# Kernel optimization log

Hardware: AMD Instinct MI355X
Metric: run time of the kernel (lower is better)

The kernel has to match this reference:

```python
import jax, jax.numpy as jnp
import numpy as np


def setup_inputs() -> dict:
    key = jax.random.key(0)
    k1, k2, k3, k4 = jax.random.split(key, 4)
    S, B = 64000, 64
    audio = jax.random.normal(k1, (S, B), dtype=jnp.float32)
    g = jax.random.uniform(k2, (S, B, 1), dtype=jnp.float32)
    twoR = jax.random.uniform(k3, (S, B, 1), dtype=jnp.float32)
    mix = jax.random.uniform(k4, (S, B, 3), dtype=jnp.float32)
    return {"audio": audio, "g": g, "twoR": twoR, "mix": mix}


def reference(audio, g, twoR, mix):
    # audio: [S, B]; g, twoR: [S, B, 1]; mix: [S, B, 3]
    S, B = audio.shape
    T = 1.0 / (1.0 + g * (g + twoR))                      # [S, B, 1]
    ones = jnp.ones_like(g)
    # Time-varying 2x2 transition matrix H[t, b] = T * [[1, -g], [g, 2Rg+1]]
    H = T[..., None] * jnp.concatenate(
        [ones, -g, g, twoR * g + 1.0], axis=-1).reshape(S, B, 2, 2)
    gHB = g * T * jnp.concatenate([ones, g], axis=-1)     # [S, B, 2]
    gHBx = gHB * audio[..., None]                         # [S, B, 2]

    def step(state, inp):
        # state: [B, 2]; Ht: [B, 2, 2]; bt: [B, 2]
        Ht, bt = inp
        Yt = bt + jnp.einsum('bij,bj->bi', Ht, state)
        return 2.0 * Yt - state, Yt

    state0 = jnp.ones((B, 2), dtype=audio.dtype)
    _, Y = jax.lax.scan(step, state0, (H, gHBx))          # Y: [S, B, 2]

    twoR2 = twoR[..., 0]                                  # [S, B]
    y_hps = audio - twoR2 * Y[..., 0] - Y[..., 1]
    y_mixed = (twoR2 * mix[..., 0] * Y[..., 0]
               + mix[..., 1] * Y[..., 1]
               + mix[..., 2] * y_hps)
    return y_mixed.T                                      # [B, S]
```

## Files before the change

kernel.cpp:

```cpp
#include <hip/hip_runtime.h>

#define S_LEN  64000
#define B_N    64
#define MCH    8
#define WPB    8
#define BSTEPS (MCH * WPB)
#define NBLK   (S_LEN / BSTEPS)
#define SC_T   1024

struct Aff { float m00, m01, m10, m11, v0, v1; };

__device__ __forceinline__ Aff aff_id() {
    Aff r; r.m00 = 1.f; r.m01 = 0.f; r.m10 = 0.f; r.m11 = 1.f; r.v0 = 0.f; r.v1 = 0.f;
    return r;
}

__device__ __forceinline__ Aff aff_comp(const Aff& X, const Aff& Y) {
    Aff r;
    r.m00 = fmaf(X.m00, Y.m00, X.m01 * Y.m10);
    r.m01 = fmaf(X.m00, Y.m01, X.m01 * Y.m11);
    r.m10 = fmaf(X.m10, Y.m00, X.m11 * Y.m10);
    r.m11 = fmaf(X.m10, Y.m01, X.m11 * Y.m11);
    r.v0  = fmaf(X.m00, Y.v0, fmaf(X.m01, Y.v1, X.v0));
    r.v1  = fmaf(X.m10, Y.v0, fmaf(X.m11, Y.v1, X.v1));
    return r;
}

__device__ __forceinline__ Aff svf_step(float g, float R, float x) {
    Aff a;
    float T  = 1.0f / fmaf(g, g + R, 1.0f);
    float gT = g * T;
    a.m00 = fmaf(2.0f, T, -1.0f);
    a.m01 = -2.0f * gT;
    a.m10 =  2.0f * gT;
    a.m11 = fmaf(2.0f, fmaf(R, gT, T), -1.0f);
    a.v0  = a.m10 * x;
    a.v1  = g * a.v0;
    return a;
}

__device__ __forceinline__ void aff_store_lds(float* p, const Aff& a) {
    p[0] = a.m00; p[1] = a.m01; p[2] = a.m10; p[3] = a.m11; p[4] = a.v0; p[5] = a.v1;
}
__device__ __forceinline__ Aff aff_load_lds(const float* p) {
    Aff a; a.m00 = p[0]; a.m01 = p[1]; a.m10 = p[2]; a.m11 = p[3]; a.v0 = p[4]; a.v1 = p[5];
    return a;
}
__device__ __forceinline__ void aff_store_g4(float4* p, const Aff& a) {
    p[0] = make_float4(a.m00, a.m01, a.m10, a.m11);
    p[1] = make_float4(a.v0,  a.v1,  0.f,   0.f);
}
__device__ __forceinline__ Aff aff_load_g4(const float4* p) {
    float4 x = p[0], y = p[1];
    Aff a; a.m00 = x.x; a.m01 = x.y; a.m10 = x.z; a.m11 = x.w; a.v0 = y.x; a.v1 = y.y;
    return a;
}

__global__ __launch_bounds__(512, 4) void k_macro(
    const float* __restrict__ audio, const float* __restrict__ g,
    const float* __restrict__ twoR, float4* __restrict__ wsMac)
{
    __shared__ float affs[WPB * B_N * 7];
    const int b   = threadIdx.x & 63;
    const int w   = threadIdx.x >> 6;
    const int blk = blockIdx.x;
    const int base = (blk * BSTEPS + w * MCH) * B_N + b;

    Aff acc = aff_id();
#pragma unroll
    for (int i = 0; i < MCH; ++i) {
        const int idx = base + i * B_N;
        acc = aff_comp(svf_step(g[idx], twoR[idx], audio[idx]), acc);
    }
    aff_store_lds(&affs[(w * B_N + b) * 7], acc);
    __syncthreads();

    if (w == 0) {
        Aff M = acc;
#pragma unroll
        for (int j = 1; j < WPB; ++j) {
            Aff A = aff_load_lds(&affs[(j * B_N + b) * 7]);
            M = aff_comp(A, M);
        }
        aff_store_g4(&wsMac[((long)b * NBLK + blk) * 2], M);
    }
}

__global__ __launch_bounds__(SC_T, 2) void k_scan(
    const float4* __restrict__ wsMac, float2* __restrict__ sIn)
{
    const int b    = blockIdx.x;
    const int t    = threadIdx.x;
    const int lane = t & 63;
    const int wave = t >> 6;

    Aff m = (t < NBLK) ? aff_load_g4(&wsMac[((long)b * NBLK + t) * 2]) : aff_id();

    Aff acc = m;
#pragma unroll
    for (int d = 1; d < 64; d <<= 1) {
        Aff o;
        o.m00 = __shfl_up(acc.m00, (unsigned)d, 64);
        o.m01 = __shfl_up(acc.m01, (unsigned)d, 64);
        o.m10 = __shfl_up(acc.m10, (unsigned)d, 64);
        o.m11 = __shfl_up(acc.m11, (unsigned)d, 64);
        o.v0  = __shfl_up(acc.v0,  (unsigned)d, 64);
        o.v1  = __shfl_up(acc.v1,  (unsigned)d, 64);
        if (lane >= d) acc = aff_comp(acc, o);
    }

    __shared__ Aff wt[SC_T / 64];
    if (lane == 63) wt[wave] = acc;
    __syncthreads();

    if (wave == 0 && lane < 16) {
        Aff a = wt[lane];
#pragma unroll
        for (int d = 1; d < 16; d <<= 1) {
            Aff o;
            o.m00 = __shfl_up(a.m00, (unsigned)d, 64);
            o.m01 = __shfl_up(a.m01, (unsigned)d, 64);
            o.m10 = __shfl_up(a.m10, (unsigned)d, 64);
            o.m11 = __shfl_up(a.m11, (unsigned)d, 64);
            o.v0  = __shfl_up(a.v0,  (unsigned)d, 64);
            o.v1  = __shfl_up(a.v1,  (unsigned)d, 64);
            if (lane >= d) a = aff_comp(a, o);
        }
        wt[lane] = a;
    }
    __syncthreads();

    if (t < NBLK) {
        Aff E;
        E.m00 = __shfl_up(acc.m00, 1u, 64);
        E.m01 = __shfl_up(acc.m01, 1u, 64);
        E.m10 = __shfl_up(acc.m10, 1u, 64);
        E.m11 = __shfl_up(acc.m11, 1u, 64);
        E.v0  = __shfl_up(acc.v0,  1u, 64);
        E.v1  = __shfl_up(acc.v1,  1u, 64);
        if (lane == 0) E = aff_id();
        if (wave > 0) E = aff_comp(E, wt[wave - 1]);

        float e0 = E.m00 + E.m01 + E.v0;
        float e1 = E.m10 + E.m11 + E.v1;
        sIn[t * B_N + b] = make_float2(e0, e1);
    }
}

__global__ __launch_bounds__(512, 4) void k_replay(
    const float* __restrict__ audio, const float* __restrict__ g,
    const float* __restrict__ twoR, const float* __restrict__ mix,
    const float2* __restrict__ sIn, float* __restrict__ out)
{
    __shared__ float lds[BSTEPS * 65];
    const int b   = threadIdx.x & 63;
    const int w   = threadIdx.x >> 6;
    const int blk = blockIdx.x;
    const int base = (blk * BSTEPS + w * MCH) * B_N + b;

    const float3* mix3 = (const float3*)mix;
    float gv[MCH], Rv[MCH], xv[MCH];
    float3 mv[MCH];
#pragma unroll
    for (int i = 0; i < MCH; ++i) {
        const int idx = base + i * B_N;
        gv[i] = g[idx]; Rv[i] = twoR[idx]; xv[i] = audio[idx];
        mv[i] = mix3[idx];
    }

    Aff acc = aff_id();
#pragma unroll
    for (int i = 0; i < MCH; ++i)
        acc = aff_comp(svf_step(gv[i], Rv[i], xv[i]), acc);
    aff_store_lds(&lds[(w * B_N + b) * 7], acc);
    __syncthreads();

    float2 sm = sIn[blk * B_N + b];
    Aff P = aff_id();
    for (int j = 0; j < w; ++j) {
        Aff A = aff_load_lds(&lds[(j * B_N + b) * 7]);
        P = aff_comp(A, P);
    }
    float s0 = fmaf(P.m00, sm.x, fmaf(P.m01, sm.y, P.v0));
    float s1 = fmaf(P.m10, sm.x, fmaf(P.m11, sm.y, P.v1));
    __syncthreads();

#pragma unroll
    for (int i = 0; i < MCH; ++i) {
        float gg = gv[i], R = Rv[i], x = xv[i];
        float T  = 1.0f / fmaf(gg, gg + R, 1.0f);
        float gT = gg * T;
        float b0 = gT * x;
        float b1 = gg * b0;
        float Y0 = fmaf(T, s0, fmaf(-gT, s1, b0));
        float Y1 = fmaf(gT, s0, fmaf(fmaf(R, gT, T), s1, b1));
        s0 = fmaf(2.0f, Y0, -s0);
        s1 = fmaf(2.0f, Y1, -s1);

        float yh = x - fmaf(R, Y0, Y1);
        float y  = fmaf(R * mv[i].x, Y0, fmaf(mv[i].y, Y1, mv[i].z * yh));

        lds[(w * MCH + i) * 65 + b] = y;
    }
    __syncthreads();

    const int col = threadIdx.x & 63;
    const int r0  = threadIdx.x >> 6;
    const int colbase = blk * BSTEPS;
#pragma unroll
    for (int r = r0; r < B_N; r += WPB) {
        out[r * S_LEN + colbase + col] = lds[col * 65 + r];
    }
}

extern "C" void kernel_launch(void* const* d_in, const int* in_sizes, int n_in,
                              void* d_out, int out_size, void* d_ws, size_t ws_size,
                              hipStream_t stream)
{
    const float* audio = (const float*)d_in[0];
    const float* g     = (const float*)d_in[1];
    const float* twoR  = (const float*)d_in[2];
    const float* mix   = (const float*)d_in[3];
    float* out = (float*)d_out;

    float4* wsMac = (float4*)d_ws;
    float2* sIn   = (float2*)(wsMac + (long)B_N * NBLK * 2);

    k_macro <<<dim3(NBLK), dim3(512), 0, stream>>>(audio, g, twoR, wsMac);
    k_scan  <<<dim3(B_N), dim3(SC_T), 0, stream>>>(wsMac, sIn);
    k_replay<<<dim3(NBLK), dim3(512), 0, stream>>>(audio, g, twoR, mix, sIn, out);
}
```

Measured before the change: 37.08 us.

## Coarsen macro blocks to 128 steps and derive half-block states in scan

The macro kernel now covers 128 timesteps per block, with each lane handling two batch columns through float2 loads. It also records a half-block prefix transform, so the scan kernel produces boundary states at 64-step granularity while scanning only 500 macro elements per batch. This halves the macro grid and cuts the scan length. The cost is extra workspace traffic for the half transforms and more serial composition work in wave 0 of the macro kernel.

```diff
diff --git a/kernel.cpp b/kernel.cpp
--- a/kernel.cpp
+++ b/kernel.cpp
@@ -3,9 +3,12 @@
 #define S_LEN  64000
 #define B_N    64
 #define MCH    8
-#define WPB    8
-#define BSTEPS (MCH * WPB)
-#define NBLK   (S_LEN / BSTEPS)
+#define CPB    16
+#define BSTEPS (MCH * CPB)
+#define NMAC   (S_LEN / BSTEPS)
+#define RSTEPS 64
+#define NREP   (S_LEN / RSTEPS)
+#define RWPB   8
 #define SC_T   1024
 
 struct Aff { float m00, m01, m10, m11, v0, v1; };
@@ -58,43 +61,56 @@
 
 __global__ __launch_bounds__(512, 4) void k_macro(
     const float* __restrict__ audio, const float* __restrict__ g,
-    const float* __restrict__ twoR, float4* __restrict__ wsMac)
-{
-    __shared__ float affs[WPB * B_N * 7];
-    const int b   = threadIdx.x & 63;
-    const int w   = threadIdx.x >> 6;
-    const int blk = blockIdx.x;
-    const int base = (blk * BSTEPS + w * MCH) * B_N + b;
-
-    Aff acc = aff_id();
+    const float* __restrict__ twoR, float4* __restrict__ wsMac,
+    float4* __restrict__ wsHalf)
+{
+    __shared__ float affs[CPB * B_N * 7];
+    const int lane = threadIdx.x & 63;
+    const int w    = threadIdx.x >> 6;
+    const int j2   = lane & 31;
+    const int h    = lane >> 5;
+    const int c    = w * 2 + h;
+    const int blk  = blockIdx.x;
+    const int base = (blk * BSTEPS + c * MCH) * B_N + 2 * j2;
+
+    Aff accA = aff_id(), accB = aff_id();
 #pragma unroll
     for (int i = 0; i < MCH; ++i) {
         const int idx = base + i * B_N;
-        acc = aff_comp(svf_step(g[idx], twoR[idx], audio[idx]), acc);
-    }
-    aff_store_lds(&affs[(w * B_N + b) * 7], acc);
+        float2 gg = *(const float2*)&g[idx];
+        float2 RR = *(const float2*)&twoR[idx];
+        float2 xx = *(const float2*)&audio[idx];
+        accA = aff_comp(svf_step(gg.x, RR.x, xx.x), accA);
+        accB = aff_comp(svf_step(gg.y, RR.y, xx.y), accB);
+    }
+    aff_store_lds(&affs[(c * B_N + 2 * j2)     * 7], accA);
+    aff_store_lds(&affs[(c * B_N + 2 * j2 + 1) * 7], accB);
     __syncthreads();
 
     if (w == 0) {
-        Aff M = acc;
-#pragma unroll
-        for (int j = 1; j < WPB; ++j) {
-            Aff A = aff_load_lds(&affs[(j * B_N + b) * 7]);
-            M = aff_comp(A, M);
+        const int b = lane;
+        Aff M = aff_load_lds(&affs[b * 7]);
+        Aff H = M;
+#pragma unroll
+        for (int j = 1; j < CPB; ++j) {
+            M = aff_comp(aff_load_lds(&affs[(j * B_N + b) * 7]), M);
+            if (j == CPB / 2 - 1) H = M;
         }
-        aff_store_g4(&wsMac[((long)b * NBLK + blk) * 2], M);
+        aff_store_g4(&wsHalf[((long)b * NMAC + blk) * 2], H);
+        aff_store_g4(&wsMac [((long)b * NMAC + blk) * 2], M);
     }
 }
 
 __global__ __launch_bounds__(SC_T, 2) void k_scan(
-    const float4* __restrict__ wsMac, float2* __restrict__ sIn)
+    const float4* __restrict__ wsMac, const float4* __restrict__ wsHalf,
+    float2* __restrict__ sIn)
 {
     const int b    = blockIdx.x;
     const int t    = threadIdx.x;
     const int lane = t & 63;
     const int wave = t >> 6;
 
-    Aff m = (t < NBLK) ? aff_load_g4(&wsMac[((long)b * NBLK + t) * 2]) : aff_id();
+    Aff m = (t < NMAC) ? aff_load_g4(&wsMac[((long)b * NMAC + t) * 2]) : aff_id();
 
     Aff acc = m;
 #pragma unroll
@@ -130,7 +146,7 @@
     }
     __syncthreads();
 
-    if (t < NBLK) {
+    if (t < NMAC) {
         Aff E;
         E.m00 = __shfl_up(acc.m00, 1u, 64);
         E.m01 = __shfl_up(acc.m01, 1u, 64);
@@ -141,9 +157,13 @@
         if (lane == 0) E = aff_id();
         if (wave > 0) E = aff_comp(E, wt[wave - 1]);
 
-        float e0 = E.m00 + E.m01 + E.v0;
-        float e1 = E.m10 + E.m11 + E.v1;
-        sIn[t * B_N + b] = make_float2(e0, e1);
+        sIn[(2 * t) * B_N + b] =
+            make_float2(E.m00 + E.m01 + E.v0, E.m10 + E.m11 + E.v1);
+
+        Aff H  = aff_load_g4(&wsHalf[((long)b * NMAC + t) * 2]);
+        Aff HE = aff_comp(H, E);
+        sIn[(2 * t + 1) * B_N + b] =
+            make_float2(HE.m00 + HE.m01 + HE.v0, HE.m10 + HE.m11 + HE.v1);
     }
 }
 
@@ -152,11 +172,11 @@
     const float* __restrict__ twoR, const float* __restrict__ mix,
     const float2* __restrict__ sIn, float* __restrict__ out)
 {
-    __shared__ float lds[BSTEPS * 65];
+    __shared__ float lds[RSTEPS * 65];
     const int b   = threadIdx.x & 63;
     const int w   = threadIdx.x >> 6;
     const int blk = blockIdx.x;
-    const int base = (blk * BSTEPS + w * MCH) * B_N + b;
+    const int base = (blk * RSTEPS + w * MCH) * B_N + b;
 
     const float3* mix3 = (const float3*)mix;
     float gv[MCH], Rv[MCH], xv[MCH];
@@ -206,9 +226,9 @@
 
     const int col = threadIdx.x & 63;
     const int r0  = threadIdx.x >> 6;
-    const int colbase = blk * BSTEPS;
-#pragma unroll
-    for (int r = r0; r < B_N; r += WPB) {
+    const int colbase = blk * RSTEPS;
+#pragma unroll
+    for (int r = r0; r < B_N; r += RWPB) {
         out[r * S_LEN + colbase + col] = lds[col * 65 + r];
     }
 }
@@ -223,10 +243,11 @@
     const float* mix   = (const float*)d_in[3];
     float* out = (float*)d_out;
 
-    float4* wsMac = (float4*)d_ws;
-    float2* sIn   = (float2*)(wsMac + (long)B_N * NBLK * 2);
-
-    k_macro <<<dim3(NBLK), dim3(512), 0, stream>>>(audio, g, twoR, wsMac);
-    k_scan  <<<dim3(B_N), dim3(SC_T), 0, stream>>>(wsMac, sIn);
-    k_replay<<<dim3(NBLK), dim3(512), 0, stream>>>(audio, g, twoR, mix, sIn, out);
-}
+    float4* wsMac  = (float4*)d_ws;
+    float4* wsHalf = wsMac + (long)B_N * NMAC * 2;
+    float2* sIn    = (float2*)(wsHalf + (long)B_N * NMAC * 2);
+
+    k_macro <<<dim3(NMAC), dim3(512), 0, stream>>>(audio, g, twoR, wsMac, wsHalf);
+    k_scan  <<<dim3(B_N), dim3(SC_T), 0, stream>>>(wsMac, wsHalf, sIn);
+    k_replay<<<dim3(NREP), dim3(512), 0, stream>>>(audio, g, twoR, mix, sIn, out);
+}
```

After: 38.26 us. 3.2% more time.

## Fuse macro, scan and replay into one cooperative kernel with grid syncs

Applied to the files above, without the earlier changes.

Merges the three phases into a single cooperative kernel that uses grid-wide syncs. Block-level affine summaries stay in LDS across phases, so the replay no longer recomputes them. Each block now covers 128 steps instead of 64, which halves the number of blocks (500, so the scan fits in 512 threads). The replay runs in two rounds of 64-column tiles, and the original three-kernel path is kept as a fallback if the cooperative launch fails. In exchange, the fused path adds two grid barriers and needs all 500 blocks to be co-resident, and only half the waves do compute in each replay round.

```diff
diff --git a/kernel.cpp b/kernel.cpp
--- a/kernel.cpp
+++ b/kernel.cpp
@@ -1,12 +1,16 @@
 #include <hip/hip_runtime.h>
+#include <hip/hip_cooperative_groups.h>
+
+namespace cg = cooperative_groups;
 
 #define S_LEN  64000
 #define B_N    64
-#define MCH    8
+#define TPB    512
 #define WPB    8
-#define BSTEPS (MCH * WPB)
+#define DSTEPS 16
+#define BSTEPS (WPB * DSTEPS)
 #define NBLK   (S_LEN / BSTEPS)
-#define SC_T   1024
+#define NMAC   NBLK
 
 struct Aff { float m00, m01, m10, m11, v0, v1; };
 
@@ -56,47 +60,43 @@
     return a;
 }
 
-__global__ __launch_bounds__(512, 4) void k_macro(
-    const float* __restrict__ audio, const float* __restrict__ g,
-    const float* __restrict__ twoR, float4* __restrict__ wsMac)
-{
-    __shared__ float affs[WPB * B_N * 7];
-    const int b   = threadIdx.x & 63;
-    const int w   = threadIdx.x >> 6;
-    const int blk = blockIdx.x;
-    const int base = (blk * BSTEPS + w * MCH) * B_N + b;
-
-    Aff acc = aff_id();
-#pragma unroll
-    for (int i = 0; i < MCH; ++i) {
-        const int idx = base + i * B_N;
-        acc = aff_comp(svf_step(g[idx], twoR[idx], audio[idx]), acc);
-    }
-    aff_store_lds(&affs[(w * B_N + b) * 7], acc);
-    __syncthreads();
-
-    if (w == 0) {
-        Aff M = acc;
-#pragma unroll
-        for (int j = 1; j < WPB; ++j) {
-            Aff A = aff_load_lds(&affs[(j * B_N + b) * 7]);
-            M = aff_comp(A, M);
-        }
-        aff_store_g4(&wsMac[((long)b * NBLK + blk) * 2], M);
-    }
-}
-
-__global__ __launch_bounds__(SC_T, 2) void k_scan(
-    const float4* __restrict__ wsMac, float2* __restrict__ sIn)
-{
-    const int b    = blockIdx.x;
-    const int t    = threadIdx.x;
-    const int lane = t & 63;
-    const int wave = t >> 6;
-
-    Aff m = (t < NBLK) ? aff_load_g4(&wsMac[((long)b * NBLK + t) * 2]) : aff_id();
-
-    Aff acc = m;
+__device__ __forceinline__ void p1_micros(float* duos,
+    const float* __restrict__ audio, const float* __restrict__ g,
+    const float* __restrict__ twoR, int blk, int tid)
+{
+    const int b = tid & 63, w = tid >> 6;
+    const int base = (blk * BSTEPS + w * DSTEPS) * B_N + b;
+    Aff lo = aff_id(), hi = aff_id();
+#pragma unroll
+    for (int i = 0; i < DSTEPS / 2; ++i) {
+        const int i0 = base + i * B_N;
+        const int i1 = base + (i + DSTEPS / 2) * B_N;
+        lo = aff_comp(svf_step(g[i0], twoR[i0], audio[i0]), lo);
+        hi = aff_comp(svf_step(g[i1], twoR[i1], audio[i1]), hi);
+    }
+    aff_store_lds(&duos[(w * B_N + b) * 7], aff_comp(hi, lo));
+}
+
+__device__ __forceinline__ void p1_write(const float* duos,
+    float4* __restrict__ wsMac, int blk, int tid)
+{
+    if (tid < B_N) {
+        const int b = tid;
+        Aff M = aff_load_lds(&duos[b * 7]);
+#pragma unroll
+        for (int j = 1; j < WPB; ++j)
+            M = aff_comp(aff_load_lds(&duos[(j * B_N + b) * 7]), M);
+        aff_store_g4(&wsMac[((long)b * NMAC + blk) * 2], M);
+    }
+}
+
+__device__ __forceinline__ void p2_scan(Aff* wt,
+    const float4* __restrict__ wsMac, float2* __restrict__ sEntry,
+    int b, int tid)
+{
+    const int lane = tid & 63, wave = tid >> 6;
+    Aff acc = (tid < NMAC) ? aff_load_g4(&wsMac[((long)b * NMAC + tid) * 2])
+                           : aff_id();
 #pragma unroll
     for (int d = 1; d < 64; d <<= 1) {
         Aff o;
@@ -108,15 +108,12 @@
         o.v1  = __shfl_up(acc.v1,  (unsigned)d, 64);
         if (lane >= d) acc = aff_comp(acc, o);
     }
-
-    __shared__ Aff wt[SC_T / 64];
     if (lane == 63) wt[wave] = acc;
     __syncthreads();
-
-    if (wave == 0 && lane < 16) {
+    if (wave == 0 && lane < WPB) {
         Aff a = wt[lane];
 #pragma unroll
-        for (int d = 1; d < 16; d <<= 1) {
+        for (int d = 1; d < WPB; d <<= 1) {
             Aff o;
             o.m00 = __shfl_up(a.m00, (unsigned)d, 64);
             o.m01 = __shfl_up(a.m01, (unsigned)d, 64);
@@ -129,8 +126,7 @@
         wt[lane] = a;
     }
     __syncthreads();
-
-    if (t < NBLK) {
+    if (tid < NMAC) {
         Aff E;
         E.m00 = __shfl_up(acc.m00, 1u, 64);
         E.m01 = __shfl_up(acc.m01, 1u, 64);
@@ -140,77 +136,110 @@
         E.v1  = __shfl_up(acc.v1,  1u, 64);
         if (lane == 0) E = aff_id();
         if (wave > 0) E = aff_comp(E, wt[wave - 1]);
-
-        float e0 = E.m00 + E.m01 + E.v0;
-        float e1 = E.m10 + E.m11 + E.v1;
-        sIn[t * B_N + b] = make_float2(e0, e1);
-    }
-}
-
-__global__ __launch_bounds__(512, 4) void k_replay(
+        sEntry[(long)tid * B_N + b] =
+            make_float2(E.m00 + E.m01 + E.v0, E.m10 + E.m11 + E.v1);
+    }
+}
+
+__device__ __forceinline__ void p3_replay(const float* duos, float* tile,
     const float* __restrict__ audio, const float* __restrict__ g,
     const float* __restrict__ twoR, const float* __restrict__ mix,
-    const float2* __restrict__ sIn, float* __restrict__ out)
-{
-    __shared__ float lds[BSTEPS * 65];
-    const int b   = threadIdx.x & 63;
-    const int w   = threadIdx.x >> 6;
-    const int blk = blockIdx.x;
-    const int base = (blk * BSTEPS + w * MCH) * B_N + b;
-
-    const float3* mix3 = (const float3*)mix;
-    float gv[MCH], Rv[MCH], xv[MCH];
-    float3 mv[MCH];
-#pragma unroll
-    for (int i = 0; i < MCH; ++i) {
-        const int idx = base + i * B_N;
-        gv[i] = g[idx]; Rv[i] = twoR[idx]; xv[i] = audio[idx];
-        mv[i] = mix3[idx];
-    }
-
-    Aff acc = aff_id();
-#pragma unroll
-    for (int i = 0; i < MCH; ++i)
-        acc = aff_comp(svf_step(gv[i], Rv[i], xv[i]), acc);
-    aff_store_lds(&lds[(w * B_N + b) * 7], acc);
-    __syncthreads();
-
-    float2 sm = sIn[blk * B_N + b];
+    const float2* __restrict__ sEntry, float* __restrict__ out,
+    int blk, int tid)
+{
+    const int b = tid & 63, w = tid >> 6;
+    float2 sm = sEntry[(long)blk * B_N + b];
     Aff P = aff_id();
-    for (int j = 0; j < w; ++j) {
-        Aff A = aff_load_lds(&lds[(j * B_N + b) * 7]);
-        P = aff_comp(A, P);
-    }
+    for (int j = 0; j < w; ++j)
+        P = aff_comp(aff_load_lds(&duos[(j * B_N + b) * 7]), P);
     float s0 = fmaf(P.m00, sm.x, fmaf(P.m01, sm.y, P.v0));
     float s1 = fmaf(P.m10, sm.x, fmaf(P.m11, sm.y, P.v1));
-    __syncthreads();
-
-#pragma unroll
-    for (int i = 0; i < MCH; ++i) {
-        float gg = gv[i], R = Rv[i], x = xv[i];
-        float T  = 1.0f / fmaf(gg, gg + R, 1.0f);
-        float gT = gg * T;
-        float b0 = gT * x;
-        float b1 = gg * b0;
-        float Y0 = fmaf(T, s0, fmaf(-gT, s1, b0));
-        float Y1 = fmaf(gT, s0, fmaf(fmaf(R, gT, T), s1, b1));
-        s0 = fmaf(2.0f, Y0, -s0);
-        s1 = fmaf(2.0f, Y1, -s1);
-
-        float yh = x - fmaf(R, Y0, Y1);
-        float y  = fmaf(R * mv[i].x, Y0, fmaf(mv[i].y, Y1, mv[i].z * yh));
-
-        lds[(w * MCH + i) * 65 + b] = y;
-    }
-    __syncthreads();
-
-    const int col = threadIdx.x & 63;
-    const int r0  = threadIdx.x >> 6;
-    const int colbase = blk * BSTEPS;
-#pragma unroll
-    for (int r = r0; r < B_N; r += WPB) {
-        out[r * S_LEN + colbase + col] = lds[col * 65 + r];
-    }
+
+    const float3* mix3 = (const float3*)mix;
+    const int base = (blk * BSTEPS + w * DSTEPS) * B_N + b;
+
+    for (int rnd = 0; rnd < 2; ++rnd) {
+        if ((w >> 2) == rnd) {
+#pragma unroll
+            for (int i = 0; i < DSTEPS; ++i) {
+                const int idx = base + i * B_N;
+                float gg = g[idx], R = twoR[idx], x = audio[idx];
+                float3 m = mix3[idx];
+                float T  = 1.0f / fmaf(gg, gg + R, 1.0f);
+                float gT = gg * T;
+                float b0 = gT * x;
+                float b1 = gg * b0;
+                float Y0 = fmaf(T, s0, fmaf(-gT, s1, b0));
+                float Y1 = fmaf(gT, s0, fmaf(fmaf(R, gT, T), s1, b1));
+                s0 = fmaf(2.0f, Y0, -s0);
+                s1 = fmaf(2.0f, Y1, -s1);
+                float yh = x - fmaf(R, Y0, Y1);
+                float y  = fmaf(R * m.x, Y0, fmaf(m.y, Y1, m.z * yh));
+                tile[((w & 3) * DSTEPS + i) * 65 + b] = y;
+            }
+        }
+        __syncthreads();
+        const int col = tid & 63, row0 = tid >> 6;
+        const int colbase = blk * BSTEPS + rnd * 64;
+#pragma unroll
+        for (int row = row0; row < B_N; row += WPB)
+            out[(long)row * S_LEN + colbase + col] = tile[col * 65 + row];
+        if (rnd == 0) __syncthreads();
+    }
+}
+
+__global__ __launch_bounds__(TPB, 4) void k_fused(
+    const float* __restrict__ audio, const float* __restrict__ g,
+    const float* __restrict__ twoR, const float* __restrict__ mix,
+    float4* __restrict__ wsMac, float2* __restrict__ sEntry,
+    float* __restrict__ out)
+{
+    __shared__ float duos[WPB * B_N * 7];
+    __shared__ float tile[64 * 65];
+    __shared__ Aff   wt[WPB];
+
+    const int tid = threadIdx.x, blk = blockIdx.x;
+
+    p1_micros(duos, audio, g, twoR, blk, tid);
+    __syncthreads();
+    p1_write(duos, wsMac, blk, tid);
+
+    cg::grid_group grid = cg::this_grid();
+    grid.sync();
+    if (blk < B_N) p2_scan(wt, wsMac, sEntry, blk, tid);
+    grid.sync();
+
+    p3_replay(duos, tile, audio, g, twoR, mix, sEntry, out, blk, tid);
+}
+
+__global__ __launch_bounds__(TPB, 4) void k_macro(
+    const float* __restrict__ audio, const float* __restrict__ g,
+    const float* __restrict__ twoR, float4* __restrict__ wsMac)
+{
+    __shared__ float duos[WPB * B_N * 7];
+    p1_micros(duos, audio, g, twoR, blockIdx.x, threadIdx.x);
+    __syncthreads();
+    p1_write(duos, wsMac, blockIdx.x, threadIdx.x);
+}
+
+__global__ __launch_bounds__(TPB, 4) void k_scan(
+    const float4* __restrict__ wsMac, float2* __restrict__ sEntry)
+{
+    __shared__ Aff wt[WPB];
+    p2_scan(wt, wsMac, sEntry, blockIdx.x, threadIdx.x);
+}
+
+__global__ __launch_bounds__(TPB, 4) void k_replay(
+    const float* __restrict__ audio, const float* __restrict__ g,
+    const float* __restrict__ twoR, const float* __restrict__ mix,
+    const float2* __restrict__ sEntry, float* __restrict__ out)
+{
+    __shared__ float duos[WPB * B_N * 7];
+    __shared__ float tile[64 * 65];
+    p1_micros(duos, audio, g, twoR, blockIdx.x, threadIdx.x);
+    __syncthreads();
+    p3_replay(duos, tile, audio, g, twoR, mix, sEntry, out,
+              blockIdx.x, threadIdx.x);
 }
 
 extern "C" void kernel_launch(void* const* d_in, const int* in_sizes, int n_in,
@@ -223,10 +252,17 @@
     const float* mix   = (const float*)d_in[3];
     float* out = (float*)d_out;
 
-    float4* wsMac = (float4*)d_ws;
-    float2* sIn   = (float2*)(wsMac + (long)B_N * NBLK * 2);
-
-    k_macro <<<dim3(NBLK), dim3(512), 0, stream>>>(audio, g, twoR, wsMac);
-    k_scan  <<<dim3(B_N), dim3(SC_T), 0, stream>>>(wsMac, sIn);
-    k_replay<<<dim3(NBLK), dim3(512), 0, stream>>>(audio, g, twoR, mix, sIn, out);
-}
+    float4* wsMac  = (float4*)d_ws;
+    float2* sEntry = (float2*)(wsMac + (long)B_N * NMAC * 2);
+
+    void* args[] = { (void*)&audio, (void*)&g, (void*)&twoR, (void*)&mix,
+                     (void*)&wsMac, (void*)&sEntry, (void*)&out };
+    hipError_t e = hipLaunchCooperativeKernel((void*)k_fused, dim3(NBLK),
+                                              dim3(TPB), args, 0, stream);
+    if (e != hipSuccess) {
+        k_macro <<<dim3(NBLK), dim3(TPB), 0, stream>>>(audio, g, twoR, wsMac);
+        k_scan  <<<dim3(B_N),  dim3(TPB), 0, stream>>>(wsMac, sEntry);
+        k_replay<<<dim3(NBLK), dim3(TPB), 0, stream>>>(audio, g, twoR, mix,
+                                                       sEntry, out);
+    }
+}
```

New measurement: 148.2 us. +299.5%, slower.

## Fuse macro-block reduction and cross-block scan via atomic ticket last-blocks

Applied to the files above, without the earlier changes.

Merges the macro-block affine reduction kernel and the per-batch scan kernel into one launch. The last 64 blocks to finish take an atomic ticket, spin until every block has published its macro affine, and then each scans one batch column with 512 threads handling two elements apiece. This removes one kernel launch and its serialization gap, at the cost of a memset for the counter, spin-waiting, and reliance on all blocks making forward progress. It also switches the output transpose stores in the replay kernel to nontemporal stores.

```diff
diff --git a/kernel.cpp b/kernel.cpp
--- a/kernel.cpp
+++ b/kernel.cpp
@@ -6,7 +6,7 @@
 #define WPB    8
 #define BSTEPS (MCH * WPB)
 #define NBLK   (S_LEN / BSTEPS)
-#define SC_T   1024
+#define KPL    2
 
 struct Aff { float m00, m01, m10, m11, v0, v1; };
 
@@ -56,13 +56,17 @@
     return a;
 }
 
-__global__ __launch_bounds__(512, 4) void k_macro(
+__global__ __launch_bounds__(512, 4) void k_macscan(
     const float* __restrict__ audio, const float* __restrict__ g,
-    const float* __restrict__ twoR, float4* __restrict__ wsMac)
+    const float* __restrict__ twoR, float4* __restrict__ wsMac,
+    float2* __restrict__ sIn, int* __restrict__ ctr)
 {
     __shared__ float affs[WPB * B_N * 7];
-    const int b   = threadIdx.x & 63;
-    const int w   = threadIdx.x >> 6;
+    __shared__ Aff wt[WPB];
+    __shared__ int shInfo;
+    const int tid = threadIdx.x;
+    const int b   = tid & 63;
+    const int w   = tid >> 6;
     const int blk = blockIdx.x;
     const int base = (blk * BSTEPS + w * MCH) * B_N + b;
 
@@ -78,45 +82,55 @@
     if (w == 0) {
         Aff M = acc;
 #pragma unroll
-        for (int j = 1; j < WPB; ++j) {
-            Aff A = aff_load_lds(&affs[(j * B_N + b) * 7]);
-            M = aff_comp(A, M);
-        }
+        for (int j = 1; j < WPB; ++j)
+            M = aff_comp(aff_load_lds(&affs[(j * B_N + b) * 7]), M);
         aff_store_g4(&wsMac[((long)b * NBLK + blk) * 2], M);
-    }
-}
-
-__global__ __launch_bounds__(SC_T, 2) void k_scan(
-    const float4* __restrict__ wsMac, float2* __restrict__ sIn)
-{
-    const int b    = blockIdx.x;
-    const int t    = threadIdx.x;
-    const int lane = t & 63;
-    const int wave = t >> 6;
-
-    Aff m = (t < NBLK) ? aff_load_g4(&wsMac[((long)b * NBLK + t) * 2]) : aff_id();
-
-    Aff acc = m;
+        __threadfence();
+    }
+    __syncthreads();
+
+    if (tid == 0)
+        shInfo = __hip_atomic_fetch_add(ctr, 1, __ATOMIC_ACQ_REL,
+                                        __HIP_MEMORY_SCOPE_AGENT);
+    __syncthreads();
+    const int ticket = shInfo;
+    if (ticket < NBLK - B_N) return;
+    const int sb = ticket - (NBLK - B_N);
+
+    if (tid == 0) {
+        while (__hip_atomic_load(ctr, __ATOMIC_ACQUIRE,
+                                 __HIP_MEMORY_SCOPE_AGENT) < NBLK)
+            __builtin_amdgcn_s_sleep(8);
+        shInfo = 1;
+    }
+    __syncthreads();
+
+    const int lane = tid & 63, wave = tid >> 6;
+    Aff c0 = aff_id(), c1 = aff_id();
+    if (2 * tid < NBLK) {
+        const float4* src = &wsMac[((long)sb * NBLK + 2 * tid) * 2];
+        c0 = aff_load_g4(src);
+        if (2 * tid + 1 < NBLK) c1 = aff_load_g4(src + 2);
+    }
+    Aff acc2 = aff_comp(c1, c0);
+
 #pragma unroll
     for (int d = 1; d < 64; d <<= 1) {
         Aff o;
-        o.m00 = __shfl_up(acc.m00, (unsigned)d, 64);
-        o.m01 = __shfl_up(acc.m01, (unsigned)d, 64);
-        o.m10 = __shfl_up(acc.m10, (unsigned)d, 64);
-        o.m11 = __shfl_up(acc.m11, (unsigned)d, 64);
-        o.v0  = __shfl_up(acc.v0,  (unsigned)d, 64);
-        o.v1  = __shfl_up(acc.v1,  (unsigned)d, 64);
-        if (lane >= d) acc = aff_comp(acc, o);
-    }
-
-    __shared__ Aff wt[SC_T / 64];
-    if (lane == 63) wt[wave] = acc;
-    __syncthreads();
-
-    if (wave == 0 && lane < 16) {
+        o.m00 = __shfl_up(acc2.m00, (unsigned)d, 64);
+        o.m01 = __shfl_up(acc2.m01, (unsigned)d, 64);
+        o.m10 = __shfl_up(acc2.m10, (unsigned)d, 64);
+        o.m11 = __shfl_up(acc2.m11, (unsigned)d, 64);
+        o.v0  = __shfl_up(acc2.v0,  (unsigned)d, 64);
+        o.v1  = __shfl_up(acc2.v1,  (unsigned)d, 64);
+        if (lane >= d) acc2 = aff_comp(acc2, o);
+    }
+    if (lane == 63) wt[wave] = acc2;
+    __syncthreads();
+    if (wave == 0 && lane < WPB) {
         Aff a = wt[lane];
 #pragma unroll
-        for (int d = 1; d < 16; d <<= 1) {
+        for (int d = 1; d < WPB; d <<= 1) {
             Aff o;
             o.m00 = __shfl_up(a.m00, (unsigned)d, 64);
             o.m01 = __shfl_up(a.m01, (unsigned)d, 64);
@@ -130,20 +144,24 @@
     }
     __syncthreads();
 
-    if (t < NBLK) {
+    if (2 * tid < NBLK) {
         Aff E;
-        E.m00 = __shfl_up(acc.m00, 1u, 64);
-        E.m01 = __shfl_up(acc.m01, 1u, 64);
-        E.m10 = __shfl_up(acc.m10, 1u, 64);
-        E.m11 = __shfl_up(acc.m11, 1u, 64);
-        E.v0  = __shfl_up(acc.v0,  1u, 64);
-        E.v1  = __shfl_up(acc.v1,  1u, 64);
+        E.m00 = __shfl_up(acc2.m00, 1u, 64);
+        E.m01 = __shfl_up(acc2.m01, 1u, 64);
+        E.m10 = __shfl_up(acc2.m10, 1u, 64);
+        E.m11 = __shfl_up(acc2.m11, 1u, 64);
+        E.v0  = __shfl_up(acc2.v0,  1u, 64);
+        E.v1  = __shfl_up(acc2.v1,  1u, 64);
         if (lane == 0) E = aff_id();
         if (wave > 0) E = aff_comp(E, wt[wave - 1]);
 
-        float e0 = E.m00 + E.m01 + E.v0;
-        float e1 = E.m10 + E.m11 + E.v1;
-        sIn[t * B_N + b] = make_float2(e0, e1);
+        sIn[(2 * tid) * B_N + sb] =
+            make_float2(E.m00 + E.m01 + E.v0, E.m10 + E.m11 + E.v1);
+        if (2 * tid + 1 < NBLK) {
+            Aff F = aff_comp(c0, E);
+            sIn[(2 * tid + 1) * B_N + sb] =
+                make_float2(F.m00 + F.m01 + F.v0, F.m10 + F.m11 + F.v1);
+        }
     }
 }
 
@@ -208,9 +226,9 @@
     const int r0  = threadIdx.x >> 6;
     const int colbase = blk * BSTEPS;
 #pragma unroll
-    for (int r = r0; r < B_N; r += WPB) {
-        out[r * S_LEN + colbase + col] = lds[col * 65 + r];
-    }
+    for (int r = r0; r < B_N; r += WPB)
+        __builtin_nontemporal_store(lds[col * 65 + r],
+                                    &out[r * S_LEN + colbase + col]);
 }
 
 extern "C" void kernel_launch(void* const* d_in, const int* in_sizes, int n_in,
@@ -225,8 +243,12 @@
 
     float4* wsMac = (float4*)d_ws;
     float2* sIn   = (float2*)(wsMac + (long)B_N * NBLK * 2);
-
-    k_macro <<<dim3(NBLK), dim3(512), 0, stream>>>(audio, g, twoR, wsMac);
-    k_scan  <<<dim3(B_N), dim3(SC_T), 0, stream>>>(wsMac, sIn);
-    k_replay<<<dim3(NBLK), dim3(512), 0, stream>>>(audio, g, twoR, mix, sIn, out);
-}
+    int*    ctr   = (int*)(sIn + (long)NBLK * B_N);
+
+    hipMemsetAsync(ctr, 0, sizeof(int), stream);
+
+    k_macscan<<<dim3(NBLK), dim3(512), 0, stream>>>(audio, g, twoR,
+                                                    wsMac, sIn, ctr);
+    k_replay <<<dim3(NBLK), dim3(512), 0, stream>>>(audio, g, twoR, mix,
+                                                    sIn, out);
+}
```

Measured after the change: 102.1 us. 2.75x slower.
